# Performance work log

Measured on AMD Instinct MI355X. Metric: run time of the kernel, lower is better.

## Reference

```python
import jax, jax.numpy as jnp
import numpy as np

B, C, W, H = 4, 256, 128, 128
BLK = 16
D = C // 8


def setup_inputs() -> dict:
    key = jax.random.key(0)
    ks = jax.random.split(key, 7)
    s = 0.05
    return {
        "x": jax.random.normal(ks[0], (B, C, W, H), jnp.float32),
        "Wq": jax.random.normal(ks[1], (D, C), jnp.float32) * s,
        "bq": jax.random.normal(ks[2], (D,), jnp.float32) * s,
        "Wk": jax.random.normal(ks[3], (D, C), jnp.float32) * s,
        "bk": jax.random.normal(ks[4], (D,), jnp.float32) * s,
        "Wv": jax.random.normal(ks[5], (C, C), jnp.float32) * s,
        "bv": jax.random.normal(ks[6], (C,), jnp.float32) * s,
        "gamma": jnp.full((1,), 0.5, jnp.float32),
    }


def reference(x, Wq, bq, Wk, bk, Wv, bv, gamma):
    Bx, Cx, Wx, Hx = x.shape
    blk = BLK
    pw = (blk - Wx % blk) % blk
    ph = (blk - Hx % blk) % blk
    xp = jnp.pad(x, ((0, 0), (0, 0), (0, pw), (0, ph))) if (pw or ph) else x
    Wp, Hp = xp.shape[2], xp.shape[3]
    nW, nH = Wp // blk, Hp // blk
    N = blk * blk
    # partition into non-overlapping blk x blk windows -> (G, C, N)
    xb = xp.reshape(Bx, Cx, nW, blk, nH, blk).transpose(0, 2, 4, 1, 3, 5)
    xb = xb.reshape(-1, Cx, N)
    # padding mask: positions whose channel-abs-sum is zero are masked out
    mask = jnp.abs(xb).sum(axis=1) > 0  # (G, N) bool
    # 1x1 convs == per-pixel linear projections
    q = jnp.einsum('dc,gcn->gnd', Wq, xb) + bq            # (G, N, D)
    k = jnp.einsum('dc,gcn->gdn', Wk, xb) + bk[:, None]   # (G, D, N)
    energy = jnp.einsum('gnd,gdm->gnm', q, k)             # (G, N, N)
    NEG = jnp.float32(-1e9)
    energy = jnp.where(mask[:, None, :], energy, NEG)  # mask keys
    energy = jnp.where(mask[:, :, None], energy, NEG)  # mask queries
    att = jax.nn.softmax(energy, axis=-1)
    v = jnp.einsum('dc,gcn->gdn', Wv, xb) + bv[:, None]   # (G, C, N)
    out = jnp.einsum('gcm,gnm->gcn', v, att)              # (G, C, N)
    out = out.reshape(Bx, nW, nH, Cx, blk, blk).transpose(0, 3, 1, 4, 2, 5)
    out = out.reshape(Bx, Cx, Wp, Hp)[:, :, :Wx, :Hx]
    out = gamma * out + x
    return out, att
```

## Files before the change

### kernel.cpp

```cpp
#include <hip/hip_runtime.h>

typedef unsigned short u16;
typedef __attribute__((ext_vector_type(8))) short short8;
typedef __attribute__((ext_vector_type(4))) short s16x4;
typedef __attribute__((ext_vector_type(4))) float f32x4;

#define CC 256
#define WW 128
#define HH 128
#define DD 32
#define NN 256
#define WH (WW * HH)
#define P8 524288
#define OUTEL 16777216

__device__ __forceinline__ u16 f2bf(float f) {
  unsigned u = __float_as_uint(f);
  return (u16)((u + 0x7FFFu + ((u >> 16) & 1u)) >> 16);
}
__device__ __forceinline__ float bf2f(u16 h) {
  return __uint_as_float(((unsigned)h) << 16);
}

__global__ __launch_bounds__(256) void k_pack(const float* __restrict__ Wq,
                                              const float* __restrict__ Wk,
                                              float* __restrict__ wqk) {
  int idx = blockIdx.x * 256 + threadIdx.x;
  int r = idx >> 8, c = idx & 255;
  float v = (r < 32) ? Wq[r * 256 + c] : Wk[(r - 32) * 256 + c];
  wqk[c * 64 + r] = v;
}

__global__ __launch_bounds__(1024, 2) void k_qk(const float* __restrict__ x,
                                                const float* __restrict__ wqk,
                                                const float* __restrict__ bq,
                                                const float* __restrict__ bk,
                                                u16* __restrict__ qk) {
  int hw = blockIdx.x;
  int g = (hw & 7) * 32 + (hw >> 3);
  int bb = g >> 6, wb = (g >> 3) & 7, hb = g & 7;
  int w0 = wb * 16, h0 = hb * 16;
  int t = threadIdx.x, ln = t & 63;
  int dg = __builtin_amdgcn_readfirstlane(t >> 6);
  int dq4 = dg & 7, is_k = dg >> 3;
  const float* xg = x + (size_t)bb * CC * WH + (size_t)(w0 + (ln >> 2)) * HH + h0 + ((4 * ln) & 15);

  float acc[4][4];
#pragma unroll
  for (int j = 0; j < 4; ++j)
#pragma unroll
    for (int i = 0; i < 4; ++i) acc[j][i] = 0.f;

#pragma unroll 2
  for (int c = 0; c < 256; ++c) {
    f32x4 xv = *(const f32x4*)(xg + (size_t)c * WH);
    f32x4 wv4 = *(const f32x4*)(wqk + c * 64 + dg * 4);
#pragma unroll
    for (int j = 0; j < 4; ++j)
#pragma unroll
      for (int i = 0; i < 4; ++i) acc[j][i] = fmaf(wv4[j], xv[i], acc[j][i]);
  }

  const float* bsrc = is_k ? bk : bq;
  float bias[4];
#pragma unroll
  for (int j = 0; j < 4; ++j) bias[j] = bsrc[dq4 * 4 + j];

  u16* ph = qk + ((size_t)((is_k << 3) + (dq4 >> 1))) * P8;
  int sub = (dq4 & 1) * 4;
#pragma unroll
  for (int i = 0; i < 4; ++i) {
    int m = 4 * ln + i;
    s16x4 hv, lv;
#pragma unroll
    for (int j = 0; j < 4; ++j) {
      float v = acc[j][i] + bias[j];
      u16 h = f2bf(v);
      hv[j] = (short)h;
      lv[j] = (short)f2bf(v - bf2f(h));
    }
    size_t ro = (size_t)(g * NN + m) * 8 + sub;
    *(s16x4*)(ph + ro) = hv;
    *(s16x4*)(ph + 4 * (size_t)P8 + ro) = lv;
  }
}

__global__ __launch_bounds__(512, 2) void k_v(const float* __restrict__ x,
                                              const float* __restrict__ Wv,
                                              const float* __restrict__ bv,
                                              u16* __restrict__ vws) {
  __shared__ u16 xb[256 * 44];
  int hw = blockIdx.x;
  int L = (hw & 7) * 64 + (hw >> 3);
  int g = L >> 1, ch = L & 1;
  int bb = g >> 6, wb = (g >> 3) & 7, hb = g & 7;
  int w0 = wb * 16, h0 = hb * 16;
  int t = threadIdx.x, ln = t & 63, wv = t >> 6;
  int cw = wv & 3, mh = wv >> 2;
  int cb = ch * 128 + cw * 32;
  int mb = mh * 128;
  const float* xg = x + (size_t)bb * CC * WH;

  f32x4 acc[2][8];
#pragma unroll
  for (int ci = 0; ci < 2; ++ci)
#pragma unroll
    for (int mt = 0; mt < 8; ++mt) acc[ci][mt] = (f32x4){0.f, 0.f, 0.f, 0.f};

  for (int ks = 0; ks < 8; ++ks) {
    int c0 = ks * 32;
    int q = ln >> 4, cl = wv * 4 + q;
#pragma unroll
    for (int it = 0; it < 4; ++it) {
      int mm = it * 64 + 4 * (ln & 15);
      f32x4 xv = *(const f32x4*)(xg + (size_t)(c0 + cl) * WH + (size_t)(w0 + (mm >> 4)) * HH +
                                 h0 + (mm & 15));
#pragma unroll
      for (int j = 0; j < 4; ++j) xb[(mm + j) * 44 + cl] = f2bf(xv[j]);
    }
    __syncthreads();

    short8 af[2];
#pragma unroll
    for (int ci = 0; ci < 2; ++ci) {
      int row = cb + ci * 16 + (ln & 15);
      const float* wp = Wv + (size_t)row * CC + c0 + (ln >> 4) * 8;
      f32x4 wa = *(const f32x4*)wp;
      f32x4 wb2 = *(const f32x4*)(wp + 4);
#pragma unroll
      for (int j = 0; j < 4; ++j) {
        af[ci][j] = (short)f2bf(wa[j]);
        af[ci][4 + j] = (short)f2bf(wb2[j]);
      }
    }
#pragma unroll
    for (int mt = 0; mt < 8; ++mt) {
      const u16* bp = &xb[(mb + mt * 16 + (ln & 15)) * 44 + (ln >> 4) * 8];
      union { short8 v; s16x4 h[2]; } bu;
      bu.h[0] = *(const s16x4*)bp;
      bu.h[1] = *(const s16x4*)(bp + 4);
#pragma unroll
      for (int ci = 0; ci < 2; ++ci)
        acc[ci][mt] = __builtin_amdgcn_mfma_f32_16x16x32_bf16(af[ci], bu.v, acc[ci][mt], 0, 0, 0);
    }
    __syncthreads();
  }

#pragma unroll
  for (int ci = 0; ci < 2; ++ci)
#pragma unroll
    for (int mt = 0; mt < 8; ++mt)
#pragma unroll
      for (int r = 0; r < 4; ++r) {
        int c = cb + ci * 16 + (ln >> 4) * 4 + r;
        int m = mb + mt * 16 + (ln & 15);
        vws[(size_t)(g * CC + c) * NN + m] = f2bf(acc[ci][mt][r] + bv[c]);
      }
}

__global__ __launch_bounds__(512, 2) void k_attn(const float* __restrict__ x,
                                                 const u16* __restrict__ qk,
                                                 const u16* __restrict__ vws,
                                                 const float* __restrict__ gamma,
                                                 float* __restrict__ dout) {
  __shared__ u16 att_lds[128 * 256];
  int hw = blockIdx.x;
  int L = (hw & 7) * 64 + (hw >> 3);
  int g = L >> 1, hf = L & 1;
  int bb = g >> 6, wb = (g >> 3) & 7, hb = g & 7;
  int w0 = wb * 16, h0 = hb * 16;
  int t = threadIdx.x, ln = t & 63, wv = t >> 6;
  float gam = gamma[0];
  float* attg = dout + (size_t)OUTEL;
  char* smem = (char*)att_lds;
  int n0 = hf * 128;
  int nt = n0 + wv * 16;
  int oct = ln >> 4;

  const u16* qb = qk + (size_t)oct * P8 + (size_t)(g * NN + nt + (ln & 15)) * 8;
  short8 ahi = *(const short8*)qb;
  short8 alo = *(const short8*)(qb + 4 * (size_t)P8);
  f32x4 e[16];
#pragma unroll
  for (int mt = 0; mt < 16; ++mt) e[mt] = (f32x4){0.f, 0.f, 0.f, 0.f};
#pragma unroll
  for (int mt = 0; mt < 16; ++mt) {
    const u16* kb = qk + (size_t)(8 + oct) * P8 + (size_t)(g * NN + mt * 16 + (ln & 15)) * 8;
    short8 bhi = *(const short8*)kb;
    short8 blo = *(const short8*)(kb + 4 * (size_t)P8);
    e[mt] = __builtin_amdgcn_mfma_f32_16x16x32_bf16(ahi, bhi, e[mt], 0, 0, 0);
    e[mt] = __builtin_amdgcn_mfma_f32_16x16x32_bf16(alo, bhi, e[mt], 0, 0, 0);
    e[mt] = __builtin_amdgcn_mfma_f32_16x16x32_bf16(ahi, blo, e[mt], 0, 0, 0);
  }

  float inv[4];
#pragma unroll
  for (int r = 0; r < 4; ++r) {
    float m0 = e[0][r];
#pragma unroll
    for (int mt = 1; mt < 16; ++mt) m0 = fmaxf(m0, e[mt][r]);
    m0 = fmaxf(m0, __shfl_xor(m0, 1));
    m0 = fmaxf(m0, __shfl_xor(m0, 2));
    m0 = fmaxf(m0, __shfl_xor(m0, 4));
    m0 = fmaxf(m0, __shfl_xor(m0, 8));
    float s = 0.f;
#pragma unroll
    for (int mt = 0; mt < 16; ++mt) {
      float p = __expf(e[mt][r] - m0);
      e[mt][r] = p;
      s += p;
    }
    s += __shfl_xor(s, 1);
    s += __shfl_xor(s, 2);
    s += __shfl_xor(s, 4);
    s += __shfl_xor(s, 8);
    inv[r] = 1.0f / s;
  }

#pragma unroll
  for (int mt = 0; mt < 16; ++mt)
#pragma unroll
    for (int r = 0; r < 4; ++r) {
      int nn = wv * 16 + (ln >> 4) * 4 + r;
      int m = mt * 16 + (ln & 15);
      int byteoff = nn * 512 + ((2 * m) ^ ((nn & 7) << 4));
      *(u16*)(smem + byteoff) = f2bf(e[mt][r] * inv[r]);
    }
  __syncthreads();

#pragma unroll
  for (int c = 0; c < 16; ++c) {
    int nn = c * 8 + (t >> 6);
    int m0 = 4 * (t & 63);
    int byteoff = nn * 512 + ((2 * m0) ^ ((nn & 7) << 4));
    s16x4 bv4 = *(const s16x4*)(smem + byteoff);
    f32x4 fv;
#pragma unroll
    for (int j = 0; j < 4; ++j) fv[j] = bf2f((u16)bv4[j]);
    *(f32x4*)(attg + (size_t)(g * NN + n0 + nn) * NN + m0) = fv;
  }

  int cbase = (wv >> 1) * 64, nb = (wv & 1) * 64;
  f32x4 o[4][4];
#pragma unroll
  for (int ci = 0; ci < 4; ++ci)
#pragma unroll
    for (int ni = 0; ni < 4; ++ni) o[ci][ni] = (f32x4){0.f, 0.f, 0.f, 0.f};

#pragma unroll
  for (int k = 0; k < 8; ++k) {
    short8 a[4];
#pragma unroll
    for (int ci = 0; ci < 4; ++ci)
      a[ci] = *(const short8*)&vws[(size_t)(g * CC + cbase + ci * 16 + (ln & 15)) * NN + k * 32 +
                                   (ln >> 4) * 8];
    short8 bf[4];
#pragma unroll
    for (int ni = 0; ni < 4; ++ni) {
      int nn = nb + ni * 16 + (ln & 15);
      int byteoff = nn * 512 + ((2 * (k * 32 + (ln >> 4) * 8)) ^ ((nn & 7) << 4));
      bf[ni] = *(const short8*)(smem + byteoff);
    }
#pragma unroll
    for (int ci = 0; ci < 4; ++ci)
#pragma unroll
      for (int ni = 0; ni < 4; ++ni)
        o[ci][ni] = __builtin_amdgcn_mfma_f32_16x16x32_bf16(a[ci], bf[ni], o[ci][ni], 0, 0, 0);
  }

#pragma unroll
  for (int ci = 0; ci < 4; ++ci)
#pragma unroll
    for (int ni = 0; ni < 4; ++ni)
#pragma unroll
      for (int r = 0; r < 4; ++r) {
        int c = cbase + ci * 16 + (ln >> 4) * 4 + r;
        int n = n0 + nb + ni * 16 + (ln & 15);
        size_t addr = (size_t)(bb * CC + c) * WH + (size_t)(w0 + (n >> 4)) * HH + h0 + (n & 15);
        dout[addr] = gam * o[ci][ni][r] + x[addr];
      }
}

extern "C" void kernel_launch(void* const* d_in, const int* in_sizes, int n_in,
                              void* d_out, int out_size, void* d_ws, size_t ws_size,
                              hipStream_t stream) {
  const float* x = (const float*)d_in[0];
  const float* Wq = (const float*)d_in[1];
  const float* bq = (const float*)d_in[2];
  const float* Wk = (const float*)d_in[3];
  const float* bk = (const float*)d_in[4];
  const float* Wv = (const float*)d_in[5];
  const float* bv = (const float*)d_in[6];
  const float* gamma = (const float*)d_in[7];
  float* out = (float*)d_out;

  float* wqk = (float*)d_ws;
  u16* qk = (u16*)((char*)d_ws + 65536);
  u16* vws = qk + 16 * (size_t)P8;

  k_pack<<<64, 256, 0, stream>>>(Wq, Wk, wqk);
  k_qk<<<256, 1024, 0, stream>>>(x, wqk, bq, bk, qk);
  k_v<<<512, 512, 0, stream>>>(x, Wv, bv, vws);
  k_attn<<<512, 512, 0, stream>>>(x, qk, vws, gamma, out);
}
```

Measured before the change: 349.7 us.

## Stage x window tiles in LDS with double buffering in QK projection kernel

The QK projection kernel now loads each 64-channel slice of the 16x16 window into shared memory cooperatively, double-buffered with register prefetch of the next slice. Previously all 16 waves re-read x directly from global memory, each wave fetching the same window data. The change cuts redundant global/L2 traffic at the cost of 128KB of LDS per block and block-wide barriers, and it drops the min-2-blocks launch bound.

```diff
diff --git a/kernel.cpp b/kernel.cpp
--- a/kernel.cpp
+++ b/kernel.cpp
@@ -31,11 +31,12 @@
   wqk[c * 64 + r] = v;
 }
 
-__global__ __launch_bounds__(1024, 2) void k_qk(const float* __restrict__ x,
-                                                const float* __restrict__ wqk,
-                                                const float* __restrict__ bq,
-                                                const float* __restrict__ bk,
-                                                u16* __restrict__ qk) {
+__global__ __launch_bounds__(1024) void k_qk(const float* __restrict__ x,
+                                             const float* __restrict__ wqk,
+                                             const float* __restrict__ bq,
+                                             const float* __restrict__ bk,
+                                             u16* __restrict__ qk) {
+  __shared__ float xs[2][64 * 256];
   int hw = blockIdx.x;
   int g = (hw & 7) * 32 + (hw >> 3);
   int bb = g >> 6, wb = (g >> 3) & 7, hb = g & 7;
@@ -43,7 +44,21 @@
   int t = threadIdx.x, ln = t & 63;
   int dg = __builtin_amdgcn_readfirstlane(t >> 6);
   int dq4 = dg & 7, is_k = dg >> 3;
-  const float* xg = x + (size_t)bb * CC * WH + (size_t)(w0 + (ln >> 2)) * HH + h0 + ((4 * ln) & 15);
+  const float* xwin = x + (size_t)bb * CC * WH + (size_t)w0 * HH + h0;
+
+  f32x4 st[4];
+#pragma unroll
+  for (int j = 0; j < 4; ++j) {
+    int lin = j * 1024 + t;
+    int c = lin >> 6, sub = lin & 63;
+    st[j] = *(const f32x4*)(xwin + (size_t)c * WH + (sub >> 2) * HH + (sub & 3) * 4);
+  }
+#pragma unroll
+  for (int j = 0; j < 4; ++j) {
+    int lin = j * 1024 + t;
+    int c = lin >> 6, sub = lin & 63;
+    *(f32x4*)&xs[0][c * 256 + sub * 4] = st[j];
+  }
 
   float acc[4][4];
 #pragma unroll
@@ -51,14 +66,37 @@
 #pragma unroll
     for (int i = 0; i < 4; ++i) acc[j][i] = 0.f;
 
-#pragma unroll 2
-  for (int c = 0; c < 256; ++c) {
-    f32x4 xv = *(const f32x4*)(xg + (size_t)c * WH);
-    f32x4 wv4 = *(const f32x4*)(wqk + c * 64 + dg * 4);
-#pragma unroll
-    for (int j = 0; j < 4; ++j)
-#pragma unroll
-      for (int i = 0; i < 4; ++i) acc[j][i] = fmaf(wv4[j], xv[i], acc[j][i]);
+  for (int s = 0; s < 4; ++s) {
+    int nxt = s + 1;
+    if (nxt < 4) {
+#pragma unroll
+      for (int j = 0; j < 4; ++j) {
+        int lin = j * 1024 + t;
+        int c = lin >> 6, sub = lin & 63;
+        st[j] = *(const f32x4*)(xwin + (size_t)(nxt * 64 + c) * WH + (sub >> 2) * HH +
+                                (sub & 3) * 4);
+      }
+    }
+    __syncthreads();
+    const float* xb = xs[s & 1];
+    const float* wp = wqk + (s * 64) * 64 + dg * 4;
+#pragma unroll 4
+    for (int cc = 0; cc < 64; ++cc) {
+      f32x4 xv = *(const f32x4*)(xb + cc * 256 + 4 * ln);
+      f32x4 wv4 = *(const f32x4*)(wp + cc * 64);
+#pragma unroll
+      for (int j = 0; j < 4; ++j)
+#pragma unroll
+        for (int i = 0; i < 4; ++i) acc[j][i] = fmaf(wv4[j], xv[i], acc[j][i]);
+    }
+    if (nxt < 4) {
+#pragma unroll
+      for (int j = 0; j < 4; ++j) {
+        int lin = j * 1024 + t;
+        int c = lin >> 6, sub = lin & 63;
+        *(f32x4*)&xs[nxt & 1][c * 256 + sub * 4] = st[j];
+      }
+    }
   }
 
   const float* bsrc = is_k ? bk : bq;
```

New measurement: 320.2 us. 8.4% less time.
